# Kernel optimization log

Hardware: AMD Instinct MI355X
Metric: run time of the kernel (lower is better)

Reference implementation:

```python
import jax, jax.numpy as jnp
import numpy as np

N_NODES = 100000
N_EDGES = 1600000
D_FEAT = 48
K = 2


def setup_inputs() -> dict:
    key = jax.random.key(0)
    k1, k2, k3, k4 = jax.random.split(key, 4)
    x = jax.random.normal(k1, (N_NODES, D_FEAT), dtype=jnp.float32)
    edge_weight = jax.random.uniform(k2, (N_EDGES,), dtype=jnp.float32)
    edge_src = jax.random.randint(k3, (N_EDGES,), 0, N_NODES, dtype=jnp.int32)
    edge_dst = jax.random.randint(k4, (N_EDGES,), 0, N_NODES, dtype=jnp.int32)
    return {"x": x, "edge_weight": edge_weight, "edge_src": edge_src, "edge_dst": edge_dst}


def _spmm(edge_weight, edge_src, edge_dst, x):
    # out[i] = sum_{e: dst[e]==i} w[e] * x[src[e]]   (sparse adj @ x)
    msgs = edge_weight[:, None] * x[edge_src]  # [E, F]
    return jax.ops.segment_sum(msgs, edge_dst, num_segments=N_NODES)


def reference(x, edge_weight, edge_src, edge_dst):
    for _ in range(K):
        x = _spmm(edge_weight, edge_src, edge_dst, x)
    return x
```

## Files before the change

kernel.cpp:

```cpp
#include <hip/hip_runtime.h>

#define N_NODES 100000
#define N_EDGES 1600000
#define D_FEAT  48

#define BKT_SHIFT 9
#define BKT_NODES (1 << BKT_SHIFT)
#define NBKT ((N_NODES + BKT_NODES - 1) / BKT_NODES)
#define EPB1 2048
#define NB1  ((N_EDGES + EPB1 - 1) / EPB1)
#define P2_CAP 9216
#define TILE_SHIFT 14
#define NTILE 8
#define KEYS (BKT_NODES * NTILE)

__device__ __forceinline__ unsigned short bf16_rn(float f) {
    unsigned u = __float_as_uint(f);
    unsigned r = (u + 0x7fffu + ((u >> 16) & 1u)) >> 16;
    return (unsigned short)r;
}
__device__ __forceinline__ float bf2f(unsigned short b) {
    return __uint_as_float(((unsigned)b) << 16);
}

__global__ void cvt_hist_kernel(const float* __restrict__ in,
                                unsigned short* __restrict__ outb,
                                const int* __restrict__ dst,
                                int* __restrict__ ccount) {
    __shared__ int cnt[NBKT];
    for (int i = threadIdx.x; i < NBKT; i += blockDim.x) cnt[i] = 0;
    __syncthreads();
    int tid = blockIdx.x * blockDim.x + threadIdx.x;
    int stride = gridDim.x * blockDim.x;
    const float4* in4 = (const float4*)in;
    ushort4* o4 = (ushort4*)outb;
    const int n4 = (N_NODES * D_FEAT) / 4;
    for (int i = tid; i < n4; i += stride) {
        float4 v = in4[i];
        ushort4 o;
        o.x = bf16_rn(v.x); o.y = bf16_rn(v.y);
        o.z = bf16_rn(v.z); o.w = bf16_rn(v.w);
        o4[i] = o;
    }
    for (int e = tid; e < N_EDGES; e += stride)
        atomicAdd(&cnt[dst[e] >> BKT_SHIFT], 1);
    __syncthreads();
    for (int i = threadIdx.x; i < NBKT; i += blockDim.x)
        if (cnt[i]) atomicAdd(&ccount[i], cnt[i]);
}

__global__ void scan196_kernel(const int* __restrict__ ccount,
                               int* __restrict__ bbase,
                               int* __restrict__ cursor,
                               int* __restrict__ row_ptr) {
    __shared__ int sdata[256];
    int t = threadIdx.x;
    int v = (t < NBKT) ? ccount[t] : 0;
    sdata[t] = v;
    __syncthreads();
    for (int off = 1; off < 256; off <<= 1) {
        int u = (t >= off) ? sdata[t - off] : 0;
        __syncthreads();
        sdata[t] += u;
        __syncthreads();
    }
    if (t < NBKT) { int ex = sdata[t] - v; bbase[t] = ex; cursor[t] = ex; }
    if (t == 0)   { bbase[NBKT] = N_EDGES; row_ptr[N_NODES] = N_EDGES; }
}

__global__ void p1_kernel(const float* __restrict__ w,
                          const int*   __restrict__ src,
                          const int*   __restrict__ dst,
                          int*         __restrict__ cursor,
                          uint2*       __restrict__ coarse) {
    __shared__ uint2 stage[EPB1];
    __shared__ unsigned char sbkt[EPB1];
    __shared__ int cnt[NBKT], base[NBKT];
    for (int i = threadIdx.x; i < NBKT; i += blockDim.x) cnt[i] = 0;
    __syncthreads();
    int e0 = blockIdx.x * EPB1;
    int n = N_EDGES - e0; if (n > EPB1) n = EPB1;
    for (int i = threadIdx.x; i < n; i += blockDim.x) {
        int e = e0 + i;
        int d = dst[e];
        int b = d >> BKT_SHIFT;
        atomicAdd(&cnt[b], 1);
        stage[i] = make_uint2((unsigned)(d & (BKT_NODES - 1)) | ((unsigned)src[e] << BKT_SHIFT),
                              (unsigned)__float_as_uint(w[e]));
        sbkt[i] = (unsigned char)b;
    }
    __syncthreads();
    for (int i = threadIdx.x; i < NBKT; i += blockDim.x) {
        int c = cnt[i];
        base[i] = c ? atomicAdd(&cursor[i], c) : 0;
        cnt[i] = 0;
    }
    __syncthreads();
    for (int i = threadIdx.x; i < n; i += blockDim.x) {
        int b = sbkt[i];
        int pos = base[b] + atomicAdd(&cnt[b], 1);
        coarse[pos] = stage[i];
    }
}

__global__ __launch_bounds__(512) void p2_kernel(const uint2* __restrict__ coarse,
                                                 const int*   __restrict__ bbase,
                                                 int2*        __restrict__ recs,
                                                 int*         __restrict__ row_ptr) {
    __shared__ uint2 sedge[P2_CAP];
    __shared__ int cnt[KEYS];
    __shared__ int ssum[512];
    int b = blockIdx.x, t = threadIdx.x;
    int lo = bbase[b], hi = bbase[b + 1];
    int m = hi - lo;
    int staged = (m < P2_CAP) ? m : P2_CAP;
    for (int i = t; i < staged; i += 512) sedge[i] = coarse[lo + i];
    for (int k = t; k < KEYS; k += 512) cnt[k] = 0;
    __syncthreads();
    for (int i = t; i < m; i += 512) {
        uint2 r = (i < staged) ? sedge[i] : coarse[lo + i];
        unsigned key = ((r.x & (BKT_NODES - 1)) << 3) | ((r.x >> BKT_SHIFT) >> TILE_SHIFT);
        atomicAdd(&cnt[key], 1);
    }
    __syncthreads();
    int base = t << 3;
    int local[NTILE];
    int s = 0;
#pragma unroll
    for (int j = 0; j < NTILE; ++j) { local[j] = s; s += cnt[base + j]; }
    ssum[t] = s;
    __syncthreads();
    for (int off = 1; off < 512; off <<= 1) {
        int u = (t >= off) ? ssum[t - off] : 0;
        __syncthreads();
        ssum[t] += u;
        __syncthreads();
    }
    int pre = lo + ssum[t] - s;
    int node = (b << BKT_SHIFT) + t;
    if (node < N_NODES) row_ptr[node] = pre;
#pragma unroll
    for (int j = 0; j < NTILE; ++j) cnt[base + j] = pre + local[j];
    __syncthreads();
    for (int i = t; i < m; i += 512) {
        uint2 r = (i < staged) ? sedge[i] : coarse[lo + i];
        unsigned src = r.x >> BKT_SHIFT;
        unsigned key = ((r.x & (BKT_NODES - 1)) << 3) | (src >> TILE_SHIFT);
        int pos = atomicAdd(&cnt[key], 1);
        recs[pos] = make_int2((int)src, (int)r.y);
    }
}

__device__ __forceinline__ void acc4(float* a, ushort4 u, float w) {
    a[0] += w * bf2f(u.x);
    a[1] += w * bf2f(u.y);
    a[2] += w * bf2f(u.z);
    a[3] += w * bf2f(u.w);
}

template <bool OUT_BF16>
__global__ void spmm_gather_b_kernel(const unsigned short* __restrict__ xb,
                                     const int2* __restrict__ recs,
                                     const int*  __restrict__ row_ptr,
                                     void* __restrict__ outv) {
    int tid = blockIdx.x * blockDim.x + threadIdx.x;
    int n = tid >> 2;
    int l = tid & 3;
    if (n >= N_NODES) return;
    int e   = row_ptr[n];
    int end = row_ptr[n + 1];
    float a0[4] = {0.f, 0.f, 0.f, 0.f};
    float a1[4] = {0.f, 0.f, 0.f, 0.f};
    float a2[4] = {0.f, 0.f, 0.f, 0.f};
    const ushort4* __restrict__ X = reinterpret_cast<const ushort4*>(xb);
    for (; e + 3 < end; e += 4) {
        int2 r0 = recs[e],     r1 = recs[e + 1];
        int2 r2 = recs[e + 2], r3 = recs[e + 3];
        const ushort4* x0 = X + (size_t)r0.x * (D_FEAT / 4);
        const ushort4* x1 = X + (size_t)r1.x * (D_FEAT / 4);
        const ushort4* x2 = X + (size_t)r2.x * (D_FEAT / 4);
        const ushort4* x3 = X + (size_t)r3.x * (D_FEAT / 4);
        ushort4 u00 = x0[l], u01 = x0[4 + l], u02 = x0[8 + l];
        ushort4 u10 = x1[l], u11 = x1[4 + l], u12 = x1[8 + l];
        ushort4 u20 = x2[l], u21 = x2[4 + l], u22 = x2[8 + l];
        ushort4 u30 = x3[l], u31 = x3[4 + l], u32 = x3[8 + l];
        float w0 = __int_as_float(r0.y), w1 = __int_as_float(r1.y);
        float w2 = __int_as_float(r2.y), w3 = __int_as_float(r3.y);
        acc4(a0, u00, w0); acc4(a1, u01, w0); acc4(a2, u02, w0);
        acc4(a0, u10, w1); acc4(a1, u11, w1); acc4(a2, u12, w1);
        acc4(a0, u20, w2); acc4(a1, u21, w2); acc4(a2, u22, w2);
        acc4(a0, u30, w3); acc4(a1, u31, w3); acc4(a2, u32, w3);
    }
    for (; e < end; ++e) {
        int2 r = recs[e];
        float we = __int_as_float(r.y);
        const ushort4* xr = X + (size_t)r.x * (D_FEAT / 4);
        acc4(a0, xr[l], we); acc4(a1, xr[4 + l], we); acc4(a2, xr[8 + l], we);
    }
    if (OUT_BF16) {
        ushort4* orow = reinterpret_cast<ushort4*>((unsigned short*)outv + (size_t)n * D_FEAT);
        ushort4 o0, o1, o2;
        o0.x = bf16_rn(a0[0]); o0.y = bf16_rn(a0[1]); o0.z = bf16_rn(a0[2]); o0.w = bf16_rn(a0[3]);
        o1.x = bf16_rn(a1[0]); o1.y = bf16_rn(a1[1]); o1.z = bf16_rn(a1[2]); o1.w = bf16_rn(a1[3]);
        o2.x = bf16_rn(a2[0]); o2.y = bf16_rn(a2[1]); o2.z = bf16_rn(a2[2]); o2.w = bf16_rn(a2[3]);
        orow[l] = o0; orow[4 + l] = o1; orow[8 + l] = o2;
    } else {
        float4* orow = reinterpret_cast<float4*>((float*)outv + (size_t)n * D_FEAT);
        orow[l]     = make_float4(a0[0], a0[1], a0[2], a0[3]);
        orow[4 + l] = make_float4(a1[0], a1[1], a1[2], a1[3]);
        orow[8 + l] = make_float4(a2[0], a2[1], a2[2], a2[3]);
    }
}

extern "C" void kernel_launch(void* const* d_in, const int* in_sizes, int n_in,
                              void* d_out, int out_size, void* d_ws, size_t ws_size,
                              hipStream_t stream) {
    const float* x    = (const float*)d_in[0];
    const float* ew   = (const float*)d_in[1];
    const int*   esrc = (const int*)d_in[2];
    const int*   edst = (const int*)d_in[3];
    float* out = (float*)d_out;

    char* ws = (char*)d_ws;
    unsigned short* xb = (unsigned short*)ws;
    ws += (((size_t)N_NODES * D_FEAT * sizeof(unsigned short)) + 15) & ~15ull;
    unsigned short* tmpb = (unsigned short*)ws;
    uint2* coarse = (uint2*)ws;
    ws += (size_t)N_EDGES * sizeof(uint2);
    int2* recs = (int2*)ws;
    ws += (size_t)N_EDGES * sizeof(int2);
    int* row_ptr = (int*)ws;
    ws += ((size_t)(N_NODES + 1) * sizeof(int) + 15) & ~15ull;
    int* ccount = (int*)ws;
    ws += ((size_t)NBKT * sizeof(int) + 15) & ~15ull;
    int* bbase = (int*)ws;
    ws += ((size_t)(NBKT + 1) * sizeof(int) + 15) & ~15ull;
    int* cursor = (int*)ws;

    dim3 blk(256);
    dim3 grid_nodes(((size_t)N_NODES * 4 + 255) / 256);

    hipMemsetAsync(ccount, 0, NBKT * sizeof(int), stream);
    cvt_hist_kernel<<<1024, blk, 0, stream>>>(x, xb, edst, ccount);
    scan196_kernel<<<1, blk, 0, stream>>>(ccount, bbase, cursor, row_ptr);
    p1_kernel<<<NB1, blk, 0, stream>>>(ew, esrc, edst, cursor, coarse);
    p2_kernel<<<NBKT, dim3(512), 0, stream>>>(coarse, bbase, recs, row_ptr);

    spmm_gather_b_kernel<true><<<grid_nodes, blk, 0, stream>>>(xb, recs, row_ptr, tmpb);
    spmm_gather_b_kernel<false><<<grid_nodes, blk, 0, stream>>>(tmpb, recs, row_ptr, out);
}
```

Measured before the change: 242.3 us.

## Sort nodes by in-degree to balance SpMM gather workload

Builds a degree histogram in the CSR build pass, scans it in descending order, and scatters node ids into an order array so the gather kernels process nodes of similar degree together. This aims to reduce wavefront divergence and tail imbalance from varying per-node edge counts. It adds two small kernels, an extra indirection per node, and scattered output writes, which lose the locality of writing rows in node order.

```diff
diff --git a/kernel.cpp b/kernel.cpp
--- a/kernel.cpp
+++ b/kernel.cpp
@@ -13,6 +13,7 @@
 #define TILE_SHIFT 14
 #define NTILE 8
 #define KEYS (BKT_NODES * NTILE)
+#define DEG_BINS 512
 
 __device__ __forceinline__ unsigned short bf16_rn(float f) {
     unsigned u = __float_as_uint(f);
@@ -106,7 +107,8 @@
 __global__ __launch_bounds__(512) void p2_kernel(const uint2* __restrict__ coarse,
                                                  const int*   __restrict__ bbase,
                                                  int2*        __restrict__ recs,
-                                                 int*         __restrict__ row_ptr) {
+                                                 int*         __restrict__ row_ptr,
+                                                 int*         __restrict__ dbin) {
     __shared__ uint2 sedge[P2_CAP];
     __shared__ int cnt[KEYS];
     __shared__ int ssum[512];
@@ -138,7 +140,11 @@
     }
     int pre = lo + ssum[t] - s;
     int node = (b << BKT_SHIFT) + t;
-    if (node < N_NODES) row_ptr[node] = pre;
+    if (node < N_NODES) {
+        row_ptr[node] = pre;
+        int d = (s < DEG_BINS) ? s : (DEG_BINS - 1);
+        atomicAdd(&dbin[d], 1);
+    }
 #pragma unroll
     for (int j = 0; j < NTILE; ++j) cnt[base + j] = pre + local[j];
     __syncthreads();
@@ -151,6 +157,34 @@
     }
 }
 
+__global__ __launch_bounds__(512) void dscan_kernel(const int* __restrict__ dbin,
+                                                    int* __restrict__ dcur) {
+    __shared__ int sdata[DEG_BINS];
+    int t = threadIdx.x;
+    int d = DEG_BINS - 1 - t;
+    int c = dbin[d];
+    sdata[t] = c;
+    __syncthreads();
+    for (int off = 1; off < DEG_BINS; off <<= 1) {
+        int u = (t >= off) ? sdata[t - off] : 0;
+        __syncthreads();
+        sdata[t] += u;
+        __syncthreads();
+    }
+    dcur[d] = sdata[t] - c;
+}
+
+__global__ void dscatter_kernel(const int* __restrict__ row_ptr,
+                                int* __restrict__ dcur,
+                                int* __restrict__ order) {
+    int n = blockIdx.x * blockDim.x + threadIdx.x;
+    if (n >= N_NODES) return;
+    int deg = row_ptr[n + 1] - row_ptr[n];
+    if (deg > DEG_BINS - 1) deg = DEG_BINS - 1;
+    int pos = atomicAdd(&dcur[deg], 1);
+    order[pos] = n;
+}
+
 __device__ __forceinline__ void acc4(float* a, ushort4 u, float w) {
     a[0] += w * bf2f(u.x);
     a[1] += w * bf2f(u.y);
@@ -162,11 +196,13 @@
 __global__ void spmm_gather_b_kernel(const unsigned short* __restrict__ xb,
                                      const int2* __restrict__ recs,
                                      const int*  __restrict__ row_ptr,
+                                     const int*  __restrict__ order,
                                      void* __restrict__ outv) {
     int tid = blockIdx.x * blockDim.x + threadIdx.x;
-    int n = tid >> 2;
+    int idx = tid >> 2;
     int l = tid & 3;
-    if (n >= N_NODES) return;
+    if (idx >= N_NODES) return;
+    int n = order[idx];
     int e   = row_ptr[n];
     int end = row_ptr[n + 1];
     float a0[4] = {0.f, 0.f, 0.f, 0.f};
@@ -231,8 +267,14 @@
     ws += (size_t)N_EDGES * sizeof(int2);
     int* row_ptr = (int*)ws;
     ws += ((size_t)(N_NODES + 1) * sizeof(int) + 15) & ~15ull;
+    int* order = (int*)ws;
+    ws += ((size_t)N_NODES * sizeof(int) + 15) & ~15ull;
     int* ccount = (int*)ws;
-    ws += ((size_t)NBKT * sizeof(int) + 15) & ~15ull;
+    ws += 256 * sizeof(int);
+    int* dbin = (int*)ws;
+    ws += DEG_BINS * sizeof(int);
+    int* dcur = (int*)ws;
+    ws += DEG_BINS * sizeof(int);
     int* bbase = (int*)ws;
     ws += ((size_t)(NBKT + 1) * sizeof(int) + 15) & ~15ull;
     int* cursor = (int*)ws;
@@ -240,12 +282,14 @@
     dim3 blk(256);
     dim3 grid_nodes(((size_t)N_NODES * 4 + 255) / 256);
 
-    hipMemsetAsync(ccount, 0, NBKT * sizeof(int), stream);
+    hipMemsetAsync(ccount, 0, (256 + DEG_BINS) * sizeof(int), stream);
     cvt_hist_kernel<<<1024, blk, 0, stream>>>(x, xb, edst, ccount);
     scan196_kernel<<<1, blk, 0, stream>>>(ccount, bbase, cursor, row_ptr);
     p1_kernel<<<NB1, blk, 0, stream>>>(ew, esrc, edst, cursor, coarse);
-    p2_kernel<<<NBKT, dim3(512), 0, stream>>>(coarse, bbase, recs, row_ptr);
-
-    spmm_gather_b_kernel<true><<<grid_nodes, blk, 0, stream>>>(xb, recs, row_ptr, tmpb);
-    spmm_gather_b_kernel<false><<<grid_nodes, blk, 0, stream>>>(tmpb, recs, row_ptr, out);
-}
+    p2_kernel<<<NBKT, dim3(512), 0, stream>>>(coarse, bbase, recs, row_ptr, dbin);
+    dscan_kernel<<<1, dim3(512), 0, stream>>>(dbin, dcur);
+    dscatter_kernel<<<(N_NODES + 255) / 256, blk, 0, stream>>>(row_ptr, dcur, order);
+
+    spmm_gather_b_kernel<true><<<grid_nodes, blk, 0, stream>>>(xb, recs, row_ptr, order, tmpb);
+    spmm_gather_b_kernel<false><<<grid_nodes, blk, 0, stream>>>(tmpb, recs, row_ptr, order, out);
+}
```

Result: slower. 821.8 us (+239.2%).
